# Optimization experiments

Measured on AMD Instinct MI355X. Metric: run time of the kernel, lower is better.

## Reference

```python
import jax, jax.numpy as jnp
import numpy as np

BETA = 0.5
CODEBOOK_STD = 0.02


def setup_inputs() -> dict:
    key = jax.random.key(0)
    k1, k2 = jax.random.split(key)
    x = jax.random.normal(k1, (16, 4096, 128), dtype=jnp.float32)
    codebook = CODEBOOK_STD * jax.random.normal(k2, (4096, 128), dtype=jnp.float32)
    return {"x": x, "codebook": codebook}


def reference(x, codebook):
    """SharedVectorQuantizer.forward (eval): tokens, STE-quantized, vq_loss.

    x:        [B, N, D] float
    codebook: [K, D]    float (embedding.weight)
    """
    B, N, D = x.shape
    flat_x = x.reshape(-1, D)  # [B*N, D]
    # Squared euclidean distances; argmin equals torch.cdist argmin.
    # d2[i,k] = ||x_i||^2 - 2 x_i . e_k + ||e_k||^2
    d2 = (
        jnp.sum(flat_x * flat_x, axis=-1, keepdims=True)
        - 2.0 * (flat_x @ codebook.T)
        + jnp.sum(codebook * codebook, axis=-1)
    )  # [B*N, K]
    tokens_flat = jnp.argmin(d2, axis=1)  # [B*N] int
    tokens = tokens_flat.reshape(B, N)
    quantized = codebook[tokens]  # [B, N, D] embedding gather

    # Losses (MSE with mean reduction)
    commitment_loss = jnp.mean((jax.lax.stop_gradient(quantized) - x) ** 2)
    embedding_loss = jnp.mean((quantized - jax.lax.stop_gradient(x)) ** 2)
    vq_loss = embedding_loss + BETA * commitment_loss

    # Straight-through estimator
    quantized_ste = x + jax.lax.stop_gradient(quantized - x)
    return tokens, quantized_ste, vq_loss
```

## Files before the change

### kernel.cpp

```cpp
#include <hip/hip_runtime.h>


#define D_ 128
#define MROWS 65536
#define KCODES 4096
#define NSUB 16
#define SUBCAP 512

#define OQ_AH    4194304
#define OQ_PAIRS 4587520
#define OQ_T1    5111808
#define OQ_T3    5177344
#define OQ_CNT   5181440
#define OQ_T3HL  5197824

typedef __attribute__((ext_vector_type(8))) short bf16x8;
typedef __attribute__((ext_vector_type(16))) float f32x16;

__device__ __forceinline__ unsigned short bf16rne(float f) {
  unsigned u = __float_as_uint(f);
  unsigned r = (u + 0x7FFFu + ((u >> 16) & 1u)) >> 16;
  return (unsigned short)r;
}
__device__ __forceinline__ float bf16tof(unsigned short h) {
  return __uint_as_float(((unsigned)h) << 16);
}

__device__ __forceinline__ void gload_lds16(const void* g, void* l) {
  __builtin_amdgcn_global_load_lds(
      (const __attribute__((address_space(1))) unsigned int*)g,
      (__attribute__((address_space(3))) unsigned int*)l, 16, 0, 0);
}

__device__ __forceinline__ float4 f4add(float4 a, float4 b) {
  return make_float4(a.x + b.x, a.y + b.y, a.z + b.z, a.w + b.w);
}
__device__ __forceinline__ float4 f4sq(float4 v) {
  return make_float4(v.x * v.x, v.y * v.y, v.z * v.z, v.w * v.w);
}

__device__ __forceinline__ float np_sumsq_row(const float4* __restrict__ r) {
  float4 W[4];
#pragma unroll
  for (int a = 0; a < 4; ++a) {
    float4 c0 = f4sq(r[0 * 4 + a]), c1 = f4sq(r[1 * 4 + a]);
    float4 c2 = f4sq(r[2 * 4 + a]), c3 = f4sq(r[3 * 4 + a]);
    float4 c4 = f4sq(r[4 * 4 + a]), c5 = f4sq(r[5 * 4 + a]);
    float4 c6 = f4sq(r[6 * 4 + a]), c7 = f4sq(r[7 * 4 + a]);
    W[a] = f4add(f4add(f4add(c0, c1), f4add(c2, c3)),
                 f4add(f4add(c4, c5), f4add(c6, c7)));
  }
  float4 U0 = f4add(W[0], W[2]);
  float4 U1 = f4add(W[1], W[3]);
  float4 T = f4add(U0, U1);
  float s0 = T.x + T.z, s1 = T.y + T.w;
  return s0 + s1;
}

__global__ __launch_bounds__(256, 2)
void k_pre(const float* __restrict__ x, const float* __restrict__ cb,
           float* __restrict__ outq, float* __restrict__ out_loss) {
  int gid = blockIdx.x * 256 + threadIdx.x;
  float* t1 = outq + OQ_T1;
  float* t3 = outq + OQ_T3;
  unsigned* t3hl = (unsigned*)(outq + OQ_T3HL);
  int* cnt = (int*)(outq + OQ_CNT);

  t1[gid] = np_sumsq_row((const float4*)(x + (size_t)gid * D_));
  if (gid < KCODES) {
    float s = np_sumsq_row((const float4*)(cb + (size_t)gid * D_));
    t3[gid] = s;
    unsigned short h = bf16rne(s);
    unsigned short l = bf16rne(s - bf16tof(h));
    t3hl[gid] = (unsigned)h | ((unsigned)l << 16);
  }
  if (gid < 64 * NSUB * 16) cnt[gid] = 0;
  if (gid == 0) out_loss[0] = 0.f;

  int u = gid;
  int ch = u >> 10, r = u & 1023;
  int s2 = r >> 6, p = r & 63;
  int kt = s2 >> 1, ct = s2 & 1;
  int kg = p >> 5, nl = p & 31;
  int code = ch * 64 + ct * 32 + nl;
  const float* src = cb + (size_t)code * D_ + (kt * 2 + kg) * 8;
  bf16x8 h8;
#pragma unroll
  for (int e = 0; e < 8; ++e) h8[e] = (short)bf16rne(src[e]);
  *(bf16x8*)((char*)(outq + OQ_AH) + (size_t)u * 16) = h8;
}

__global__ __launch_bounds__(256, 3)
void k_big(const float* __restrict__ x, const unsigned* __restrict__ t3hl,
           float* __restrict__ outq) {
  __shared__ char lds[2][16384];
  const int tid = threadIdx.x;
  const int lane = tid & 63;
  const int w = tid >> 6;
  const int kg = lane >> 5, nl = lane & 31;
  const int rb = blockIdx.x >> 1, cs = blockIdx.x & 1;
  const int row0 = rb * 256 + w * 64;

  const char* AhB = (const char*)(outq + OQ_AH);
  float* cm = outq;

  bf16x8 xh[2][8];
#pragma unroll
  for (int xt = 0; xt < 2; ++xt)
#pragma unroll
    for (int kt = 0; kt < 8; ++kt) {
      const float* src =
          x + (size_t)(row0 + xt * 32 + nl) * D_ + (kt * 2 + kg) * 8;
      float f[8];
      *(float4*)(f) = *(const float4*)(src);
      *(float4*)(f + 4) = *(const float4*)(src + 4);
      bf16x8 h;
#pragma unroll
      for (int e = 0; e < 8; ++e) h[e] = (short)bf16rne(f[e]);
      xh[xt][kt] = h;
    }

  bf16x8 bneg = 0;
  if (kg == 0) { bneg[0] = (short)0xBF00; bneg[1] = (short)0xBF00; }

#define STAGE(c, buf)                                                         \
  {                                                                           \
    const char* sAh = AhB + (size_t)(c) * 16384;                              \
    _Pragma("unroll")                                                         \
    for (int i4 = 0; i4 < 4; ++i4) {                                          \
      int ub = i4 * 256 + w * 64;                                             \
      gload_lds16(sAh + (size_t)(ub + lane) * 16, (buf) + ub * 16);           \
    }                                                                         \
  }

  STAGE(cs * 32 + 0, lds[0]);
  unsigned v0 = t3hl[(cs * 32) * 64 + nl];
  unsigned v1 = t3hl[(cs * 32) * 64 + 32 + nl];
  __syncthreads();

  int b = 0;
  for (int it = 0; it < 32; ++it) {
    int ch = cs * 32 + it;
    char* cur = lds[b];
    if (it < 31) STAGE(ch + 1, lds[b ^ 1]);

    unsigned nv0 = 0, nv1 = 0;
    if (it < 31) {
      nv0 = t3hl[(ch + 1) * 64 + nl];
      nv1 = t3hl[(ch + 1) * 64 + 32 + nl];
    }

    bf16x8 s0 = 0, s1 = 0;
    if (kg == 0) {
      s0[0] = (short)(v0 & 0xFFFFu); s0[1] = (short)(v0 >> 16);
      s1[0] = (short)(v1 & 0xFFFFu); s1[1] = (short)(v1 >> 16);
    }

    f32x16 a00 = 0, a01 = 0, a10 = 0, a11 = 0;
    a00 = __builtin_amdgcn_mfma_f32_32x32x16_bf16(s0, bneg, a00, 0, 0, 0);
    a01 = __builtin_amdgcn_mfma_f32_32x32x16_bf16(s0, bneg, a01, 0, 0, 0);
    a10 = __builtin_amdgcn_mfma_f32_32x32x16_bf16(s1, bneg, a10, 0, 0, 0);
    a11 = __builtin_amdgcn_mfma_f32_32x32x16_bf16(s1, bneg, a11, 0, 0, 0);
#pragma unroll
    for (int kt = 0; kt < 8; ++kt) {
      bf16x8 e0 = *(const bf16x8*)(cur + ((kt * 2 + 0) * 64 + lane) * 16);
      bf16x8 e1 = *(const bf16x8*)(cur + ((kt * 2 + 1) * 64 + lane) * 16);
      a00 = __builtin_amdgcn_mfma_f32_32x32x16_bf16(e0, xh[0][kt], a00, 0, 0, 0);
      a01 = __builtin_amdgcn_mfma_f32_32x32x16_bf16(e0, xh[1][kt], a01, 0, 0, 0);
      a10 = __builtin_amdgcn_mfma_f32_32x32x16_bf16(e1, xh[0][kt], a10, 0, 0, 0);
      a11 = __builtin_amdgcn_mfma_f32_32x32x16_bf16(e1, xh[1][kt], a11, 0, 0, 0);
    }

    float m0 = -3.4e38f, m1 = -3.4e38f;
#pragma unroll
    for (int e = 0; e < 16; ++e) {
      m0 = fmaxf(m0, fmaxf(a00[e], a10[e]));
      m1 = fmaxf(m1, fmaxf(a01[e], a11[e]));
    }
    m0 = fmaxf(m0, __shfl_xor(m0, 32, 64));
    m1 = fmaxf(m1, __shfl_xor(m1, 32, 64));
    float mv = (kg == 0) ? m0 : m1;
    size_t caddr = (size_t)ch * MROWS + row0 + kg * 32 + nl;

    __syncthreads();
    cm[caddr] = mv;
    v0 = nv0; v1 = nv1;
    b ^= 1;
  }
#undef STAGE
}

__global__ __launch_bounds__(256, 4)
void k_cand(const float* __restrict__ cm, int* __restrict__ cnt,
            int* __restrict__ pairs, unsigned long long* __restrict__ keys,
            float dlt) {
  __shared__ float wmax[4][64];
  __shared__ float thrs[64];
  const int tid = threadIdx.x, lane = tid & 63, w = tid >> 6;
  const int r = blockIdx.x * 64 + lane;
  const int sub = blockIdx.x & (NSUB - 1);
  float v[16];
#pragma unroll
  for (int i = 0; i < 16; ++i) v[i] = cm[(size_t)(w * 16 + i) * MROWS + r];
  float m = v[0];
#pragma unroll
  for (int i = 1; i < 16; ++i) m = fmaxf(m, v[i]);
  wmax[w][lane] = m;
  __syncthreads();
  if (w == 0) {
    float A = fmaxf(fmaxf(wmax[0][lane], wmax[1][lane]),
                    fmaxf(wmax[2][lane], wmax[3][lane]));
    thrs[lane] = A - dlt;
    keys[r] = ~0ull;
  }
  __syncthreads();
  float thr = thrs[lane];
#pragma unroll
  for (int i = 0; i < 16; ++i) {
    if (v[i] >= thr) {
      int ch = w * 16 + i;
      int slot = ch * NSUB + sub;
      int s = atomicAdd(cnt + slot * 16, 1);
      if (s < SUBCAP) pairs[slot * SUBCAP + s] = r;
    }
  }
}

__global__ __launch_bounds__(256, 4)
void k_exact(const float* __restrict__ x, const float* __restrict__ cb,
             const int* __restrict__ cnt, const int* __restrict__ pairs,
             const float* __restrict__ t1, const float* __restrict__ t3,
             unsigned long long* __restrict__ keys) {
  __shared__ float elds[32 * 65 * 4];
  __shared__ float xlds[4][D_];
  int ch = blockIdx.x >> 4, sub = blockIdx.x & (NSUB - 1);
  int tid = threadIdx.x, lane = tid & 63, wid = tid >> 6;
#pragma unroll
  for (int it2 = 0; it2 < 8; ++it2) {
    int u = it2 * 256 + tid;
    int c = u >> 5, d4 = u & 31;
    float4 v = *(const float4*)(cb + ((size_t)ch * 64 + c) * D_ + d4 * 4);
    *(float4*)(elds + (d4 * 65 + c) * 4) = v;
  }
  float t3v = t3[ch * 64 + lane];
  __syncthreads();
  int slot = ch * NSUB + sub;
  int n = cnt[slot * 16]; if (n > SUBCAP) n = SUBCAP;
  const int* lst = pairs + slot * SUBCAP;
  for (int idx = wid; idx < n; idx += 4) {
    int row = lst[idx];
    *(float2*)(&xlds[wid][lane * 2]) = *(const float2*)(x + (size_t)row * D_ + lane * 2);
    asm volatile("s_waitcnt lgkmcnt(0)" ::: "memory");
    float acc = 0.f;
    float t1r = t1[row];
#pragma unroll 8
    for (int d4 = 0; d4 < 32; ++d4) {
      float4 xv = *(const float4*)(&xlds[wid][d4 * 4]);
      float4 ev = *(const float4*)(elds + (d4 * 65 + lane) * 4);
      acc = __builtin_fmaf(xv.x, ev.x, acc);
      acc = __builtin_fmaf(xv.y, ev.y, acc);
      acc = __builtin_fmaf(xv.z, ev.z, acc);
      acc = __builtin_fmaf(xv.w, ev.w, acc);
    }
    float s = __builtin_fmaf(-2.f, acc, t1r) + t3v;
    unsigned u32 = __float_as_uint(s);
    u32 = u32 ^ (unsigned)(((int)u32 >> 31) | 0x80000000);
    unsigned long long key =
        ((unsigned long long)u32 << 12) | (unsigned)(ch * 64 + lane);
#pragma unroll
    for (int off = 1; off < 64; off <<= 1) {
      unsigned long long o = __shfl_xor(key, off, 64);
      key = o < key ? o : key;
    }
    if (lane == 0) atomicMin(keys + row, key);
  }
}

__global__ __launch_bounds__(256, 8)
void k_gather(const float* __restrict__ x, const float* __restrict__ cb,
              const unsigned long long* __restrict__ keys,
              float* __restrict__ tok_f, float* __restrict__ outq,
              float* __restrict__ partial) {
  int idx = blockIdx.x * 256 + threadIdx.x;
  int row = idx >> 5;
  int d4 = idx & 31;
  int t = (int)(keys[row] & 0xFFFull);
  if (d4 == 0) tok_f[row] = (float)t;
  float4 q = ((const float4*)(cb + (size_t)t * D_))[d4];
  float4 xv = ((const float4*)x)[idx];
  ((float4*)outq)[idx] = q;
  float dx = q.x - xv.x, dy = q.y - xv.y, dz = q.z - xv.z, dw = q.w - xv.w;
  float s = dx * dx + dy * dy + dz * dz + dw * dw;
#pragma unroll
  for (int off = 1; off < 64; off <<= 1) s += __shfl_xor(s, off, 64);
  __shared__ float red[4];
  int lane = threadIdx.x & 63, w = threadIdx.x >> 6;
  if (lane == 0) red[w] = s;
  __syncthreads();
  if (threadIdx.x == 0)
    partial[blockIdx.x] = red[0] + red[1] + red[2] + red[3];
}

__global__ __launch_bounds__(256, 1)
void k_loss(const float* __restrict__ partial, float* __restrict__ out_loss,
            float scale) {
  int i = blockIdx.x * 256 + threadIdx.x;
  float s = partial[i];
#pragma unroll
  for (int off = 1; off < 64; off <<= 1) s += __shfl_xor(s, off, 64);
  __shared__ float red[4];
  int lane = threadIdx.x & 63, w = threadIdx.x >> 6;
  if (lane == 0) red[w] = s;
  __syncthreads();
  if (threadIdx.x == 0)
    atomicAdd(out_loss, (red[0] + red[1] + red[2] + red[3]) * scale);
}

extern "C" void kernel_launch(void* const* d_in, const int* in_sizes, int n_in,
                              void* d_out, int out_size, void* d_ws, size_t ws_size,
                              hipStream_t stream) {
  const float* x = (const float*)d_in[0];
  const float* cb = (const float*)d_in[1];

  float* out_tok = (float*)d_out;
  float* outq = (float*)d_out + MROWS;
  float* out_loss = (float*)d_out + MROWS + (size_t)MROWS * D_;

  unsigned long long* keys = (unsigned long long*)d_ws;
  float* part = (float*)((char*)d_ws + 524288);

  float* t3 = outq + OQ_T3;
  float* t1 = outq + OQ_T1;
  unsigned* t3hl = (unsigned*)(outq + OQ_T3HL);
  int* cnt = (int*)(outq + OQ_CNT);
  int* pairs = (int*)(outq + OQ_PAIRS);

  k_pre<<<MROWS / 256, 256, 0, stream>>>(x, cb, outq, out_loss);
  k_big<<<(MROWS / 256) * 2, 256, 0, stream>>>(x, t3hl, outq);
  k_cand<<<MROWS / 64, 256, 0, stream>>>(outq, cnt, pairs, keys, 8e-3f);
  k_exact<<<64 * NSUB, 256, 0, stream>>>(x, cb, cnt, pairs, t1, t3, keys);
  const int gB = (MROWS * (D_ / 4)) / 256;
  k_gather<<<gB, 256, 0, stream>>>(x, cb, keys, out_tok, outq, part);
  k_loss<<<32, 256, 0, stream>>>(part, out_loss,
                                 1.5f / (float)((size_t)MROWS * D_));
}
```

Measured before the change: 184.2 us.

## Split row sum-of-squares across 4 lanes and fold loss reduction into gather

The x-row sum-of-squares in k_pre is now computed by four lanes per row and combined with shuffles. The grid grows to 1024 blocks, which gives more parallel loads and better coalescing. The separate k_loss kernel is removed: the last k_gather block, detected with an atomic done-counter and thread fences, sums all partials and writes the loss. This saves one launch but adds an atomic and a serial tail in one block.

Measured after the change: 580.0 us. 215% more time.

```diff
diff --git a/kernel.cpp b/kernel.cpp
--- a/kernel.cpp
+++ b/kernel.cpp
@@ -59,14 +59,37 @@
 
 __global__ __launch_bounds__(256, 2)
 void k_pre(const float* __restrict__ x, const float* __restrict__ cb,
-           float* __restrict__ outq, float* __restrict__ out_loss) {
+           float* __restrict__ outq, float* __restrict__ out_loss,
+           unsigned* __restrict__ donecnt) {
   int gid = blockIdx.x * 256 + threadIdx.x;
   float* t1 = outq + OQ_T1;
   float* t3 = outq + OQ_T3;
   unsigned* t3hl = (unsigned*)(outq + OQ_T3HL);
   int* cnt = (int*)(outq + OQ_CNT);
 
-  t1[gid] = np_sumsq_row((const float4*)(x + (size_t)gid * D_));
+  {
+    int row = gid >> 2, a = gid & 3;
+    const float4* r4 = (const float4*)(x + (size_t)row * D_);
+    float4 c0 = f4sq(r4[0 * 4 + a]), c1 = f4sq(r4[1 * 4 + a]);
+    float4 c2 = f4sq(r4[2 * 4 + a]), c3 = f4sq(r4[3 * 4 + a]);
+    float4 c4 = f4sq(r4[4 * 4 + a]), c5 = f4sq(r4[5 * 4 + a]);
+    float4 c6 = f4sq(r4[6 * 4 + a]), c7 = f4sq(r4[7 * 4 + a]);
+    float4 wv = f4add(f4add(f4add(c0, c1), f4add(c2, c3)),
+                      f4add(f4add(c4, c5), f4add(c6, c7)));
+    int lb = (threadIdx.x & 63) & ~3;
+    int sp = lb + (a | 2);
+    float4 wp;
+    wp.x = __shfl(wv.x, sp, 64); wp.y = __shfl(wv.y, sp, 64);
+    wp.z = __shfl(wv.z, sp, 64); wp.w = __shfl(wv.w, sp, 64);
+    float4 U = f4add(wv, wp);
+    float4 u1;
+    u1.x = __shfl(U.x, lb + 1, 64); u1.y = __shfl(U.y, lb + 1, 64);
+    u1.z = __shfl(U.z, lb + 1, 64); u1.w = __shfl(U.w, lb + 1, 64);
+    float4 T = f4add(U, u1);
+    float res = (T.x + T.z) + (T.y + T.w);
+    if (a == 0) t1[row] = res;
+  }
+
   if (gid < KCODES) {
     float s = np_sumsq_row((const float4*)(cb + (size_t)gid * D_));
     t3[gid] = s;
@@ -75,19 +98,21 @@
     t3hl[gid] = (unsigned)h | ((unsigned)l << 16);
   }
   if (gid < 64 * NSUB * 16) cnt[gid] = 0;
-  if (gid == 0) out_loss[0] = 0.f;
-
-  int u = gid;
-  int ch = u >> 10, r = u & 1023;
-  int s2 = r >> 6, p = r & 63;
-  int kt = s2 >> 1, ct = s2 & 1;
-  int kg = p >> 5, nl = p & 31;
-  int code = ch * 64 + ct * 32 + nl;
-  const float* src = cb + (size_t)code * D_ + (kt * 2 + kg) * 8;
-  bf16x8 h8;
-#pragma unroll
-  for (int e = 0; e < 8; ++e) h8[e] = (short)bf16rne(src[e]);
-  *(bf16x8*)((char*)(outq + OQ_AH) + (size_t)u * 16) = h8;
+  if (gid == 0) { out_loss[0] = 0.f; donecnt[0] = 0u; }
+
+  if (gid < 64 * 1024) {
+    int u = gid;
+    int ch = u >> 10, r = u & 1023;
+    int s2 = r >> 6, p = r & 63;
+    int kt = s2 >> 1, ct = s2 & 1;
+    int kg = p >> 5, nl = p & 31;
+    int code = ch * 64 + ct * 32 + nl;
+    const float* src = cb + (size_t)code * D_ + (kt * 2 + kg) * 8;
+    bf16x8 h8;
+#pragma unroll
+    for (int e = 0; e < 8; ++e) h8[e] = (short)bf16rne(src[e]);
+    *(bf16x8*)((char*)(outq + OQ_AH) + (size_t)u * 16) = h8;
+  }
 }
 
 __global__ __launch_bounds__(256, 3)
@@ -280,7 +305,8 @@
 void k_gather(const float* __restrict__ x, const float* __restrict__ cb,
               const unsigned long long* __restrict__ keys,
               float* __restrict__ tok_f, float* __restrict__ outq,
-              float* __restrict__ partial) {
+              float* __restrict__ partial, unsigned* __restrict__ donecnt,
+              float* __restrict__ out_loss, float scale, int gB) {
   int idx = blockIdx.x * 256 + threadIdx.x;
   int row = idx >> 5;
   int d4 = idx & 31;
@@ -294,26 +320,28 @@
 #pragma unroll
   for (int off = 1; off < 64; off <<= 1) s += __shfl_xor(s, off, 64);
   __shared__ float red[4];
+  __shared__ int last;
   int lane = threadIdx.x & 63, w = threadIdx.x >> 6;
   if (lane == 0) red[w] = s;
   __syncthreads();
-  if (threadIdx.x == 0)
+  if (threadIdx.x == 0) {
     partial[blockIdx.x] = red[0] + red[1] + red[2] + red[3];
-}
-
-__global__ __launch_bounds__(256, 1)
-void k_loss(const float* __restrict__ partial, float* __restrict__ out_loss,
-            float scale) {
-  int i = blockIdx.x * 256 + threadIdx.x;
-  float s = partial[i];
-#pragma unroll
-  for (int off = 1; off < 64; off <<= 1) s += __shfl_xor(s, off, 64);
-  __shared__ float red[4];
-  int lane = threadIdx.x & 63, w = threadIdx.x >> 6;
-  if (lane == 0) red[w] = s;
-  __syncthreads();
-  if (threadIdx.x == 0)
-    atomicAdd(out_loss, (red[0] + red[1] + red[2] + red[3]) * scale);
+    __threadfence();
+    unsigned d = atomicAdd(donecnt, 1u);
+    __threadfence();
+    last = (d == (unsigned)(gB - 1));
+  }
+  __syncthreads();
+  if (last) {
+    float acc = 0.f;
+    for (int i = threadIdx.x; i < gB; i += 256) acc += partial[i];
+#pragma unroll
+    for (int off = 1; off < 64; off <<= 1) acc += __shfl_xor(acc, off, 64);
+    if (lane == 0) red[w] = acc;
+    __syncthreads();
+    if (threadIdx.x == 0)
+      out_loss[0] = (red[0] + red[1] + red[2] + red[3]) * scale;
+  }
 }
 
 extern "C" void kernel_launch(void* const* d_in, const int* in_sizes, int n_in,
@@ -328,6 +356,7 @@
 
   unsigned long long* keys = (unsigned long long*)d_ws;
   float* part = (float*)((char*)d_ws + 524288);
+  unsigned* donecnt = (unsigned*)((char*)d_ws + 557056);
 
   float* t3 = outq + OQ_T3;
   float* t1 = outq + OQ_T1;
@@ -335,12 +364,12 @@
   int* cnt = (int*)(outq + OQ_CNT);
   int* pairs = (int*)(outq + OQ_PAIRS);
 
-  k_pre<<<MROWS / 256, 256, 0, stream>>>(x, cb, outq, out_loss);
+  k_pre<<<1024, 256, 0, stream>>>(x, cb, outq, out_loss, donecnt);
   k_big<<<(MROWS / 256) * 2, 256, 0, stream>>>(x, t3hl, outq);
   k_cand<<<MROWS / 64, 256, 0, stream>>>(outq, cnt, pairs, keys, 8e-3f);
   k_exact<<<64 * NSUB, 256, 0, stream>>>(x, cb, cnt, pairs, t1, t3, keys);
   const int gB = (MROWS * (D_ / 4)) / 256;
-  k_gather<<<gB, 256, 0, stream>>>(x, cb, keys, out_tok, outq, part);
-  k_loss<<<32, 256, 0, stream>>>(part, out_loss,
-                                 1.5f / (float)((size_t)MROWS * D_));
-}
+  k_gather<<<gB, 256, 0, stream>>>(x, cb, keys, out_tok, outq, part,
+                                   donecnt, out_loss,
+                                   1.5f / (float)((size_t)MROWS * D_), gB);
+}
```
